# Kernel tuning notes

Hardware: AMD Instinct MI355X
Metric: run time of the kernel (lower is better)

The kernel has to match this reference:

```python
import jax, jax.numpy as jnp
import numpy as np

NOPE = 128          # qk_nope_head_dim
ROPE = 64           # qk_rope_head_dim
KV_LORA = 512       # kv_lora_rank
SCALE = (KV_LORA + ROPE) ** (-0.5)


def setup_inputs() -> dict:
    key = jax.random.key(0)
    k1, k2, k3, k4, k5 = jax.random.split(key, 5)
    T, H, K, S = 512, 128, 512, 8192
    q = jax.random.normal(k1, (T, H, NOPE + ROPE), dtype=jnp.float32)
    kv_cache = jax.random.normal(k2, (S, KV_LORA + ROPE), dtype=jnp.float32)
    topk_indices = jax.random.randint(k3, (T, K), 0, S, dtype=jnp.int32)
    k_b_proj_trans = jax.random.normal(k4, (H, KV_LORA, NOPE), dtype=jnp.float32) * 0.02
    v_b_proj = jax.random.normal(k5, (H, 128, KV_LORA), dtype=jnp.float32) * 0.02
    return {"q": q, "kv_cache": kv_cache, "topk_indices": topk_indices,
            "k_b_proj_trans": k_b_proj_trans, "v_b_proj": v_b_proj}


def reference(q, kv_cache, topk_indices, k_b_proj_trans, v_b_proj):
    # q: [T, H, 192]; kv_cache: [S, 576]; topk_indices: [T, K]
    q_nope, q_rope = q[..., :NOPE], q[..., NOPE:]
    # bmm_out(q_nope_t, k_b_proj_trans.transpose(1,2)): [T,H,128] x [H,512,128] -> [T,H,512]
    q_lat = jnp.einsum('thd,hkd->thk', q_nope, k_b_proj_trans)
    q_concat = jnp.concatenate([q_lat, q_rope], axis=-1)        # [T, H, 576]
    # sparse MLA: gather selected latent KV per token
    kv_sel = kv_cache[topk_indices]                              # [T, K, 576]
    scores = jnp.einsum('thc,tkc->thk', q_concat, kv_sel) * SCALE
    p = jax.nn.softmax(scores, axis=-1)                          # [T, H, K]
    attn_lat = jnp.einsum('thk,tkc->thc', p, kv_sel[..., :KV_LORA])  # [T, H, 512]
    # bmm_out(attn_lat_t, v_b_proj.transpose(1,2)): [T,H,512] x [H,512,128] -> [T,H,128]
    out = jnp.einsum('thc,hvc->thv', attn_lat, v_b_proj)
    return out
```

## Files before the change

### kernel.cpp

```cpp
#include <hip/hip_runtime.h>
#include <stdint.h>


#define SCALE 0.041666666666666664f

typedef __bf16 bf16x8 __attribute__((ext_vector_type(8)));
typedef float floatx4 __attribute__((ext_vector_type(4)));
typedef unsigned int uint32x2 __attribute__((ext_vector_type(2)));
typedef unsigned int uint32x4 __attribute__((ext_vector_type(4)));

static __device__ __forceinline__ unsigned short f2bf(float f) {
  unsigned int u = __builtin_bit_cast(unsigned int, f);
  u += 0x7FFF + ((u >> 16) & 1);
  return (unsigned short)(u >> 16);
}
static __device__ __forceinline__ float bf2f(unsigned short h) {
  unsigned int u = ((unsigned int)h) << 16;
  return __builtin_bit_cast(float, u);
}
static __device__ __forceinline__ unsigned int pack2(float lo, float hi) {
  return (unsigned int)f2bf(lo) | ((unsigned int)f2bf(hi) << 16);
}
static __device__ __forceinline__ void ldsdma16(const void* g, void* l) {
  __builtin_amdgcn_global_load_lds(
      (const __attribute__((address_space(1))) void*)g,
      (__attribute__((address_space(3))) void*)l, 16, 0, 0);
}
static __device__ __forceinline__ void issue_fence() {
  asm volatile("" ::: "memory");
  __builtin_amdgcn_sched_barrier(0);
}
static __device__ __forceinline__ unsigned int lds_addr(const void* p) {
  return (unsigned int)(unsigned long long)(
      (__attribute__((address_space(3))) const void*)p);
}
#define TR64(dst, addr, OFF) \
  asm volatile("ds_read_b64_tr_b16 %0, %1 offset:" OFF : "=v"(dst) : "v"(addr))

static __device__ __forceinline__ void stage8_f32(const float* __restrict__ src,
                                                  unsigned short* dst) {
  const float4* s4 = reinterpret_cast<const float4*>(src);
  float4 v0 = s4[0], v1 = s4[1];
  uint4 o;
  o.x = pack2(v0.x, v0.y); o.y = pack2(v0.z, v0.w);
  o.z = pack2(v1.x, v1.y); o.w = pack2(v1.z, v1.w);
  *reinterpret_cast<uint4*>(dst) = o;
}

static __device__ __forceinline__ void mfma_4x4(const unsigned short* As,
                                                const unsigned short* Bs,
                                                int wm, int wn, int l15, int quad,
                                                floatx4 acc[4][4]) {
  bf16x8 af[4], bfr[4];
#pragma unroll
  for (int i = 0; i < 4; ++i)
    af[i] = *reinterpret_cast<const bf16x8*>(&As[(wm + i * 16 + l15) * 32 + quad * 8]);
#pragma unroll
  for (int j = 0; j < 4; ++j)
    bfr[j] = *reinterpret_cast<const bf16x8*>(&Bs[(wn + j * 16 + l15) * 32 + quad * 8]);
#pragma unroll
  for (int i = 0; i < 4; ++i)
#pragma unroll
    for (int j = 0; j < 4; ++j)
      acc[i][j] = __builtin_amdgcn_mfma_f32_16x16x32_bf16(af[i], bfr[j], acc[i][j], 0, 0, 0);
}

__global__ void prep(const float* __restrict__ kv, unsigned short* __restrict__ kvb,
                     const float* __restrict__ q, unsigned short* __restrict__ qc2) {
  int b = blockIdx.x;
  if (b < 4608) {
    int i = b * 256 + threadIdx.x;
    float4 v = reinterpret_cast<const float4*>(kv)[i];
    ushort4 o;
    o.x = f2bf(v.x); o.y = f2bf(v.y); o.z = f2bf(v.z); o.w = f2bf(v.w);
    reinterpret_cast<ushort4*>(kvb)[i] = o;
  } else {
    int i = (b - 4608) * 256 + threadIdx.x;
    int r = i & 63;
    int th = i >> 6;
    int t = th >> 7, h = th & 127;
    qc2[(((size_t)t * 18 + 16 + (r >> 5)) * 128 + h) * 32 + (r & 31)] =
        f2bf(q[(size_t)th * 192 + 128 + r] * SCALE);
  }
}

__global__ __launch_bounds__(256) void qlat_gemm(const float* __restrict__ q,
                                                 const float* __restrict__ kb,
                                                 unsigned short* __restrict__ qc2) {
  const int h = blockIdx.x;
  const int tm = (blockIdx.y & 3) * 128;
  const int tn = (blockIdx.y >> 2) * 128;
  __shared__ __align__(16) unsigned short As[128 * 32];
  __shared__ __align__(16) unsigned short Bs[128 * 32];
  const int tid = threadIdx.x;
  const int lane = tid & 63, wave = tid >> 6;
  const int wm = (wave & 1) * 64, wn = (wave >> 1) * 64;
  const int l15 = lane & 15, quad = lane >> 4;
  const int r0 = tid >> 2, cg = tid & 3;
  const float* a0 = q + ((size_t)(tm + r0) * 128 + h) * 192 + cg * 8;
  const float* a1 = q + ((size_t)(tm + r0 + 64) * 128 + h) * 192 + cg * 8;
  const float* b0 = kb + ((size_t)h * 512 + tn + r0) * 128 + cg * 8;
  const float* b1 = b0 + (size_t)64 * 128;
  floatx4 acc[4][4] = {};
  for (int ks = 0; ks < 4; ++ks) {
    stage8_f32(a0 + ks * 32, &As[tid * 8]);
    stage8_f32(a1 + ks * 32, &As[2048 + tid * 8]);
    stage8_f32(b0 + ks * 32, &Bs[tid * 8]);
    stage8_f32(b1 + ks * 32, &Bs[2048 + tid * 8]);
    __syncthreads();
    mfma_4x4(As, Bs, wm, wn, l15, quad, acc);
    __syncthreads();
  }
#pragma unroll
  for (int i = 0; i < 4; ++i) {
    const int row = wm + i * 16 + quad * 4;
#pragma unroll
    for (int j = 0; j < 4; ++j) {
      const int c = tn + wn + j * 16 + l15;
      const int ks2 = c >> 5, kk = c & 31;
#pragma unroll
      for (int r = 0; r < 4; ++r) {
        const int t = tm + row + r;
        qc2[(((size_t)t * 18 + ks2) * 128 + h) * 32 + kk] = f2bf(acc[i][j][r] * SCALE);
      }
    }
  }
}

__global__ __launch_bounds__(256) void scores_gemm(const unsigned short* __restrict__ qc2,
                                                   const unsigned short* __restrict__ kvb,
                                                   const int* __restrict__ topk,
                                                   unsigned short* __restrict__ P) {
  const int t = blockIdx.x;
  const int tn = blockIdx.y * 128;
  __shared__ __align__(16) unsigned short Bs[3][128 * 32];
  const int tid = threadIdx.x;
  const int lane = tid & 63, wave = tid >> 6;
  const int wm = (wave & 1) * 64, wn = (wave >> 1) * 64;
  const int l15 = lane & 15, quad = lane >> 4;
  const int r0 = tid >> 2, cg = tid & 3;
  const int idx0 = topk[t * 512 + tn + r0];
  const int idx1 = topk[t * 512 + tn + r0 + 64];
  const unsigned short* b0 = kvb + (size_t)idx0 * 576 + cg * 8;
  const unsigned short* b1 = kvb + (size_t)idx1 * 576 + cg * 8;
  const unsigned short* aab =
      qc2 + ((size_t)t * 2304 + wm + l15) * 32 + quad * 8;
  floatx4 acc[4][4] = {};
  ldsdma16(b0, &Bs[0][tid * 8]);
  ldsdma16(b1, &Bs[0][2048 + tid * 8]);
  ldsdma16(b0 + 32, &Bs[1][tid * 8]);
  ldsdma16(b1 + 32, &Bs[1][2048 + tid * 8]);
  issue_fence();
  bf16x8 af[4], an[4];
#pragma unroll
  for (int i = 0; i < 4; ++i)
    af[i] = *reinterpret_cast<const bf16x8*>(aab + i * 512);
  int bi = 0, bn = 2;
  for (int ks = 0; ks < 18; ++ks) {
    asm volatile("s_waitcnt vmcnt(6)" ::: "memory");
    __builtin_amdgcn_s_barrier();
    if (ks < 16) {
      ldsdma16(b0 + (ks + 2) * 32, &Bs[bn][tid * 8]);
      ldsdma16(b1 + (ks + 2) * 32, &Bs[bn][2048 + tid * 8]);
      issue_fence();
    }
    if (ks < 17) {
#pragma unroll
      for (int i = 0; i < 4; ++i)
        an[i] = *reinterpret_cast<const bf16x8*>(
            aab + (size_t)(ks + 1) * 4096 + i * 512);
    }
    bf16x8 bfr[4];
#pragma unroll
    for (int j = 0; j < 4; ++j)
      bfr[j] = *reinterpret_cast<const bf16x8*>(
          &Bs[bi][(wn + j * 16 + l15) * 32 + quad * 8]);
#pragma unroll
    for (int i = 0; i < 4; ++i)
#pragma unroll
      for (int j = 0; j < 4; ++j)
        acc[i][j] =
            __builtin_amdgcn_mfma_f32_16x16x32_bf16(af[i], bfr[j], acc[i][j], 0, 0, 0);
    __builtin_amdgcn_s_barrier();
#pragma unroll
    for (int i = 0; i < 4; ++i) af[i] = an[i];
    bi = bi == 2 ? 0 : bi + 1;
    bn = bn == 2 ? 0 : bn + 1;
  }
#pragma unroll
  for (int i = 0; i < 4; ++i) {
    const int row = wm + i * 16 + quad * 4;
#pragma unroll
    for (int j = 0; j < 4; ++j) {
      const int col = tn + wn + j * 16 + l15;
#pragma unroll
      for (int r = 0; r < 4; ++r)
        P[((size_t)t * 128 + row + r) * 512 + col] = f2bf(acc[i][j][r]);
    }
  }
}

__global__ __launch_bounds__(256) void softmax_rows(const unsigned short* __restrict__ Pin,
                                                    unsigned short* __restrict__ P2) {
  const int row = blockIdx.x * 4 + (threadIdx.x >> 6);
  const int t = row >> 7, h = row & 127;
  const int lane = threadIdx.x & 63;
  const unsigned short* rp = Pin + (size_t)row * 512 + lane * 8;
  uint4 raw = *reinterpret_cast<const uint4*>(rp);
  unsigned int w[4] = {raw.x, raw.y, raw.z, raw.w};
  float f[8];
  float mx = -1e30f;
#pragma unroll
  for (int i = 0; i < 8; ++i) {
    f[i] = bf2f((unsigned short)((w[i >> 1] >> ((i & 1) * 16)) & 0xFFFF));
    mx = fmaxf(mx, f[i]);
  }
#pragma unroll
  for (int off = 32; off; off >>= 1) mx = fmaxf(mx, __shfl_xor(mx, off, 64));
  float s = 0.f;
#pragma unroll
  for (int i = 0; i < 8; ++i) { f[i] = __expf(f[i] - mx); s += f[i]; }
#pragma unroll
  for (int off = 32; off; off >>= 1) s += __shfl_xor(s, off, 64);
  const float inv = 1.0f / s;
  uint4 o;
  o.x = pack2(f[0] * inv, f[1] * inv);
  o.y = pack2(f[2] * inv, f[3] * inv);
  o.z = pack2(f[4] * inv, f[5] * inv);
  o.w = pack2(f[6] * inv, f[7] * inv);
  unsigned short* wp =
      P2 + (((size_t)t * 16 + (lane >> 2)) * 128 + h) * 32 + (lane & 3) * 8;
  *reinterpret_cast<uint4*>(wp) = o;
}

__global__ __launch_bounds__(512) void attn_gemm(const unsigned short* __restrict__ P2,
                                                 const unsigned short* __restrict__ kvb,
                                                 const int* __restrict__ topk,
                                                 unsigned short* __restrict__ alat2) {
  const int t = blockIdx.x;
  __shared__ __align__(16) unsigned short St[3][32 * 512];
  const int tid = threadIdx.x;
  const int lane = tid & 63, wave = tid >> 6;
  const int wm = (wave >> 2) * 64;
  const int wc = wave & 3;
  const int l15 = lane & 15, quad = lane >> 4;
  const int keyBase = (tid >> 8) * 4 + ((tid >> 1) & 3);
  const int cA = ((tid >> 3) & 31) * 16 + (tid & 1) * 8;
  const int* tkrow = topk + t * 512;
  const unsigned short* a_base =
      P2 + ((size_t)t * 16 * 128 + wm + l15) * 32 + quad * 8;
  const unsigned int tra0 = lds_addr(&St[0][0]) + quad * 8192 + wc * 1024 + l15 * 8;
  floatx4 acc[4][8] = {};
  bf16x8 a_cur[4], a_nxt[4];
  int ip0, ip1, ip2, ip3;
  {
#pragma unroll
    for (int d = 0; d < 4; ++d) {
      const int k0 = tkrow[d * 8 + keyBase];
      ldsdma16(kvb + (size_t)k0 * 576 + cA, &St[0][d * 4096 + tid * 8]);
    }
#pragma unroll
    for (int i = 0; i < 4; ++i)
      a_cur[i] = *reinterpret_cast<const bf16x8*>(a_base + (size_t)i * 16 * 32);
    ip0 = tkrow[64 + 0 * 8 + keyBase];
    ip1 = tkrow[64 + 1 * 8 + keyBase];
    ip2 = tkrow[64 + 2 * 8 + keyBase];
    ip3 = tkrow[64 + 3 * 8 + keyBase];
    issue_fence();
#pragma unroll
    for (int d = 0; d < 4; ++d) {
      const int k1 = tkrow[32 + d * 8 + keyBase];
      ldsdma16(kvb + (size_t)k1 * 576 + cA, &St[1][d * 4096 + tid * 8]);
    }
  }
  int sti = 0, stp = 2;
  for (int ks = 0; ks < 16; ++ks) {
    asm volatile("s_waitcnt vmcnt(4)" ::: "memory");
    __builtin_amdgcn_s_barrier();
    const unsigned int tra = tra0 + sti * 32768;
    uint32x2 rl0, rl1, rl2, rl3, rl4, rl5, rl6, rl7;
    uint32x2 rh0, rh1, rh2, rh3, rh4, rh5, rh6, rh7;
    TR64(rl0, tra, "0");    TR64(rh0, tra, "4096");
    TR64(rl1, tra, "128");  TR64(rh1, tra, "4224");
    TR64(rl2, tra, "256");  TR64(rh2, tra, "4352");
    TR64(rl3, tra, "384");  TR64(rh3, tra, "4480");
    TR64(rl4, tra, "512");  TR64(rh4, tra, "4608");
    TR64(rl5, tra, "640");  TR64(rh5, tra, "4736");
    TR64(rl6, tra, "768");  TR64(rh6, tra, "4864");
    TR64(rl7, tra, "896");  TR64(rh7, tra, "4992");
    if (ks < 15) {
#pragma unroll
      for (int i = 0; i < 4; ++i)
        a_nxt[i] = *reinterpret_cast<const bf16x8*>(
            a_base + ((size_t)(ks + 1) * 128 + i * 16) * 32);
    }
    if (ks < 14) {
      const int d0 = ip0, d1 = ip1, d2 = ip2, d3 = ip3;
      if (ks < 13) {
        ip0 = tkrow[(ks + 3) * 32 + 0 * 8 + keyBase];
        ip1 = tkrow[(ks + 3) * 32 + 1 * 8 + keyBase];
        ip2 = tkrow[(ks + 3) * 32 + 2 * 8 + keyBase];
        ip3 = tkrow[(ks + 3) * 32 + 3 * 8 + keyBase];
      }
      issue_fence();
      ldsdma16(kvb + (size_t)d0 * 576 + cA, &St[stp][0 * 4096 + tid * 8]);
      ldsdma16(kvb + (size_t)d1 * 576 + cA, &St[stp][1 * 4096 + tid * 8]);
      ldsdma16(kvb + (size_t)d2 * 576 + cA, &St[stp][2 * 4096 + tid * 8]);
      ldsdma16(kvb + (size_t)d3 * 576 + cA, &St[stp][3 * 4096 + tid * 8]);
    }
    asm volatile("s_waitcnt lgkmcnt(0)");
    __builtin_amdgcn_sched_barrier(0);
    bf16x8 bfr[8];
    {
      uint32x4 w;
      w.x = rl0.x; w.y = rl0.y; w.z = rh0.x; w.w = rh0.y; bfr[0] = __builtin_bit_cast(bf16x8, w);
      w.x = rl1.x; w.y = rl1.y; w.z = rh1.x; w.w = rh1.y; bfr[1] = __builtin_bit_cast(bf16x8, w);
      w.x = rl2.x; w.y = rl2.y; w.z = rh2.x; w.w = rh2.y; bfr[2] = __builtin_bit_cast(bf16x8, w);
      w.x = rl3.x; w.y = rl3.y; w.z = rh3.x; w.w = rh3.y; bfr[3] = __builtin_bit_cast(bf16x8, w);
      w.x = rl4.x; w.y = rl4.y; w.z = rh4.x; w.w = rh4.y; bfr[4] = __builtin_bit_cast(bf16x8, w);
      w.x = rl5.x; w.y = rl5.y; w.z = rh5.x; w.w = rh5.y; bfr[5] = __builtin_bit_cast(bf16x8, w);
      w.x = rl6.x; w.y = rl6.y; w.z = rh6.x; w.w = rh6.y; bfr[6] = __builtin_bit_cast(bf16x8, w);
      w.x = rl7.x; w.y = rl7.y; w.z = rh7.x; w.w = rh7.y; bfr[7] = __builtin_bit_cast(bf16x8, w);
    }
#pragma unroll
    for (int i = 0; i < 4; ++i)
#pragma unroll
      for (int j = 0; j < 8; ++j)
        acc[i][j] =
            __builtin_amdgcn_mfma_f32_16x16x32_bf16(a_cur[i], bfr[j], acc[i][j], 0, 0, 0);
#pragma unroll
    for (int i = 0; i < 4; ++i) a_cur[i] = a_nxt[i];
    sti = sti == 2 ? 0 : sti + 1;
    stp = stp == 2 ? 0 : stp + 1;
  }
#pragma unroll
  for (int i = 0; i < 4; ++i) {
    const int row = wm + i * 16 + quad * 4;
#pragma unroll
    for (int j = 0; j < 8; ++j) {
      const int c = wc * 128 + j * 16 + l15;
      const int ks2 = c >> 5, kk = c & 31;
#pragma unroll
      for (int r = 0; r < 4; ++r)
        alat2[(((size_t)(row + r) * 16 + ks2) * 512 + t) * 32 + kk] =
            f2bf(acc[i][j][r]);
    }
  }
}

__global__ __launch_bounds__(256) void out_gemm(const unsigned short* __restrict__ alat2,
                                                const float* __restrict__ vb,
                                                float* __restrict__ out) {
  const int h = blockIdx.x;
  const int tm = blockIdx.y * 128;
  __shared__ __align__(16) unsigned short Bs[128 * 32];
  const int tid = threadIdx.x;
  const int lane = tid & 63, wave = tid >> 6;
  const int wm = (wave & 1) * 64, wn = (wave >> 1) * 64;
  const int l15 = lane & 15, quad = lane >> 4;
  const int r0 = tid >> 2, cg = tid & 3;
  const unsigned short* aab =
      alat2 + ((size_t)h * 8192 + tm + wm + l15) * 32 + quad * 8;
  const float* b0 = vb + ((size_t)h * 128 + r0) * 512 + cg * 8;
  const float* b1 = b0 + (size_t)64 * 512;
  floatx4 acc[4][4] = {};
  for (int ks = 0; ks < 16; ++ks) {
    stage8_f32(b0 + ks * 32, &Bs[tid * 8]);
    stage8_f32(b1 + ks * 32, &Bs[2048 + tid * 8]);
    __syncthreads();
    bf16x8 af[4], bfr[4];
#pragma unroll
    for (int i = 0; i < 4; ++i)
      af[i] = *reinterpret_cast<const bf16x8*>(
          aab + (size_t)ks * 16384 + i * 512);
#pragma unroll
    for (int j = 0; j < 4; ++j)
      bfr[j] = *reinterpret_cast<const bf16x8*>(
          &Bs[(wn + j * 16 + l15) * 32 + quad * 8]);
#pragma unroll
    for (int i = 0; i < 4; ++i)
#pragma unroll
      for (int j = 0; j < 4; ++j)
        acc[i][j] =
            __builtin_amdgcn_mfma_f32_16x16x32_bf16(af[i], bfr[j], acc[i][j], 0, 0, 0);
    __syncthreads();
  }
#pragma unroll
  for (int i = 0; i < 4; ++i) {
    const int row = wm + i * 16 + quad * 4;
#pragma unroll
    for (int j = 0; j < 4; ++j) {
      const int col = wn + j * 16 + l15;
#pragma unroll
      for (int r = 0; r < 4; ++r) {
        const int t = tm + row + r;
        out[((size_t)t * 128 + h) * 128 + col] = acc[i][j][r];
      }
    }
  }
}

extern "C" void kernel_launch(void* const* d_in, const int* in_sizes, int n_in,
                              void* d_out, int out_size, void* d_ws, size_t ws_size,
                              hipStream_t stream) {
  const float* q = (const float*)d_in[0];
  const float* kv = (const float*)d_in[1];
  const int* topk = (const int*)d_in[2];
  const float* kb = (const float*)d_in[3];
  const float* vb = (const float*)d_in[4];
  float* out = (float*)d_out;

  char* ws = (char*)d_ws;
  unsigned short* kvb = (unsigned short*)ws;
  unsigned short* qc2 = (unsigned short*)(ws + 9437184);
  unsigned short* P = (unsigned short*)(ws + 9437184 + 75497472);
  unsigned short* P2 = qc2;
  unsigned short* alat2 = P;

  prep<<<dim3(20992), dim3(256), 0, stream>>>(kv, kvb, q, qc2);
  qlat_gemm<<<dim3(128, 16), dim3(256), 0, stream>>>(q, kb, qc2);
  scores_gemm<<<dim3(512, 4), dim3(256), 0, stream>>>(qc2, kvb, topk, P);
  softmax_rows<<<dim3(16384), dim3(256), 0, stream>>>(P, P2);
  attn_gemm<<<dim3(512), dim3(512), 0, stream>>>(P2, kvb, topk, alat2);
  out_gemm<<<dim3(128, 4), dim3(256), 0, stream>>>(alat2, vb, out);
}
```

Measured before the change: 384.6 us.

## Fuse score GEMM with softmax into one per-token kernel

The scores GEMM now uses one 512-thread block per token that covers all 512 selected keys, instead of four 128-key blocks. The row softmax is done in registers, with cross-wave max and sum reductions through small LDS arrays, and the normalized bf16 probabilities are written straight into the layout attn_gemm expects. This removes the separate softmax kernel and the write and re-read of the full bf16 score matrix, and it drops the trailing barrier in the K loop. In exchange it uses about 100KB of LDS per block, doubles the accumulator registers per lane and launches far fewer blocks, which may lower occupancy and latency hiding.

```diff
diff --git a/kernel.cpp b/kernel.cpp
--- a/kernel.cpp
+++ b/kernel.cpp
@@ -127,29 +127,42 @@
   }
 }
 
-__global__ __launch_bounds__(256) void scores_gemm(const unsigned short* __restrict__ qc2,
-                                                   const unsigned short* __restrict__ kvb,
-                                                   const int* __restrict__ topk,
-                                                   unsigned short* __restrict__ P) {
+__global__ __launch_bounds__(512) void scores_fused(const unsigned short* __restrict__ qc2,
+                                                    const unsigned short* __restrict__ kvb,
+                                                    const int* __restrict__ topk,
+                                                    unsigned short* __restrict__ P2) {
   const int t = blockIdx.x;
-  const int tn = blockIdx.y * 128;
-  __shared__ __align__(16) unsigned short Bs[3][128 * 32];
+  __shared__ __align__(16) unsigned short Bs[3][512 * 32];
+  __shared__ __align__(16) float redmx[128][4];
+  __shared__ __align__(16) float redsm[128][4];
   const int tid = threadIdx.x;
   const int lane = tid & 63, wave = tid >> 6;
-  const int wm = (wave & 1) * 64, wn = (wave >> 1) * 64;
+  const int wm2 = (wave >> 2) * 64;
+  const int wkn = (wave & 3) * 128;
   const int l15 = lane & 15, quad = lane >> 4;
-  const int r0 = tid >> 2, cg = tid & 3;
-  const int idx0 = topk[t * 512 + tn + r0];
-  const int idx1 = topk[t * 512 + tn + r0 + 64];
-  const unsigned short* b0 = kvb + (size_t)idx0 * 576 + cg * 8;
-  const unsigned short* b1 = kvb + (size_t)idx1 * 576 + cg * 8;
+  const int keyD = tid >> 2;
+  const int cD = (tid & 3) * 8;
+  const int* tkrow = topk + t * 512;
+  const int gi0 = tkrow[0 * 128 + keyD];
+  const int gi1 = tkrow[1 * 128 + keyD];
+  const int gi2 = tkrow[2 * 128 + keyD];
+  const int gi3 = tkrow[3 * 128 + keyD];
+  const unsigned short* g0 = kvb + (size_t)gi0 * 576 + cD;
+  const unsigned short* g1 = kvb + (size_t)gi1 * 576 + cD;
+  const unsigned short* g2 = kvb + (size_t)gi2 * 576 + cD;
+  const unsigned short* g3 = kvb + (size_t)gi3 * 576 + cD;
   const unsigned short* aab =
-      qc2 + ((size_t)t * 2304 + wm + l15) * 32 + quad * 8;
-  floatx4 acc[4][4] = {};
-  ldsdma16(b0, &Bs[0][tid * 8]);
-  ldsdma16(b1, &Bs[0][2048 + tid * 8]);
-  ldsdma16(b0 + 32, &Bs[1][tid * 8]);
-  ldsdma16(b1 + 32, &Bs[1][2048 + tid * 8]);
+      qc2 + ((size_t)t * 2304 + wm2 + l15) * 32 + quad * 8;
+  floatx4 acc[4][8] = {};
+  ldsdma16(g0, &Bs[0][0 * 4096 + tid * 8]);
+  ldsdma16(g1, &Bs[0][1 * 4096 + tid * 8]);
+  ldsdma16(g2, &Bs[0][2 * 4096 + tid * 8]);
+  ldsdma16(g3, &Bs[0][3 * 4096 + tid * 8]);
+  issue_fence();
+  ldsdma16(g0 + 32, &Bs[1][0 * 4096 + tid * 8]);
+  ldsdma16(g1 + 32, &Bs[1][1 * 4096 + tid * 8]);
+  ldsdma16(g2 + 32, &Bs[1][2 * 4096 + tid * 8]);
+  ldsdma16(g3 + 32, &Bs[1][3 * 4096 + tid * 8]);
   issue_fence();
   bf16x8 af[4], an[4];
 #pragma unroll
@@ -157,11 +170,13 @@
     af[i] = *reinterpret_cast<const bf16x8*>(aab + i * 512);
   int bi = 0, bn = 2;
   for (int ks = 0; ks < 18; ++ks) {
-    asm volatile("s_waitcnt vmcnt(6)" ::: "memory");
+    asm volatile("s_waitcnt vmcnt(8)" ::: "memory");
     __builtin_amdgcn_s_barrier();
     if (ks < 16) {
-      ldsdma16(b0 + (ks + 2) * 32, &Bs[bn][tid * 8]);
-      ldsdma16(b1 + (ks + 2) * 32, &Bs[bn][2048 + tid * 8]);
+      ldsdma16(g0 + (ks + 2) * 32, &Bs[bn][0 * 4096 + tid * 8]);
+      ldsdma16(g1 + (ks + 2) * 32, &Bs[bn][1 * 4096 + tid * 8]);
+      ldsdma16(g2 + (ks + 2) * 32, &Bs[bn][2 * 4096 + tid * 8]);
+      ldsdma16(g3 + (ks + 2) * 32, &Bs[bn][3 * 4096 + tid * 8]);
       issue_fence();
     }
     if (ks < 17) {
@@ -170,67 +185,80 @@
         an[i] = *reinterpret_cast<const bf16x8*>(
             aab + (size_t)(ks + 1) * 4096 + i * 512);
     }
-    bf16x8 bfr[4];
-#pragma unroll
-    for (int j = 0; j < 4; ++j)
+    bf16x8 bfr[8];
+#pragma unroll
+    for (int j = 0; j < 8; ++j)
       bfr[j] = *reinterpret_cast<const bf16x8*>(
-          &Bs[bi][(wn + j * 16 + l15) * 32 + quad * 8]);
+          &Bs[bi][(wkn + j * 16 + l15) * 32 + quad * 8]);
 #pragma unroll
     for (int i = 0; i < 4; ++i)
 #pragma unroll
-      for (int j = 0; j < 4; ++j)
+      for (int j = 0; j < 8; ++j)
         acc[i][j] =
             __builtin_amdgcn_mfma_f32_16x16x32_bf16(af[i], bfr[j], acc[i][j], 0, 0, 0);
-    __builtin_amdgcn_s_barrier();
 #pragma unroll
     for (int i = 0; i < 4; ++i) af[i] = an[i];
     bi = bi == 2 ? 0 : bi + 1;
     bn = bn == 2 ? 0 : bn + 1;
   }
-#pragma unroll
-  for (int i = 0; i < 4; ++i) {
-    const int row = wm + i * 16 + quad * 4;
-#pragma unroll
-    for (int j = 0; j < 4; ++j) {
-      const int col = tn + wn + j * 16 + l15;
-#pragma unroll
-      for (int r = 0; r < 4; ++r)
-        P[((size_t)t * 128 + row + r) * 512 + col] = f2bf(acc[i][j][r]);
-    }
-  }
-}
-
-__global__ __launch_bounds__(256) void softmax_rows(const unsigned short* __restrict__ Pin,
-                                                    unsigned short* __restrict__ P2) {
-  const int row = blockIdx.x * 4 + (threadIdx.x >> 6);
-  const int t = row >> 7, h = row & 127;
-  const int lane = threadIdx.x & 63;
-  const unsigned short* rp = Pin + (size_t)row * 512 + lane * 8;
-  uint4 raw = *reinterpret_cast<const uint4*>(rp);
-  unsigned int w[4] = {raw.x, raw.y, raw.z, raw.w};
-  float f[8];
-  float mx = -1e30f;
-#pragma unroll
-  for (int i = 0; i < 8; ++i) {
-    f[i] = bf2f((unsigned short)((w[i >> 1] >> ((i & 1) * 16)) & 0xFFFF));
-    mx = fmaxf(mx, f[i]);
-  }
-#pragma unroll
-  for (int off = 32; off; off >>= 1) mx = fmaxf(mx, __shfl_xor(mx, off, 64));
-  float s = 0.f;
-#pragma unroll
-  for (int i = 0; i < 8; ++i) { f[i] = __expf(f[i] - mx); s += f[i]; }
-#pragma unroll
-  for (int off = 32; off; off >>= 1) s += __shfl_xor(s, off, 64);
-  const float inv = 1.0f / s;
-  uint4 o;
-  o.x = pack2(f[0] * inv, f[1] * inv);
-  o.y = pack2(f[2] * inv, f[3] * inv);
-  o.z = pack2(f[4] * inv, f[5] * inv);
-  o.w = pack2(f[6] * inv, f[7] * inv);
-  unsigned short* wp =
-      P2 + (((size_t)t * 16 + (lane >> 2)) * 128 + h) * 32 + (lane & 3) * 8;
-  *reinterpret_cast<uint4*>(wp) = o;
+  float fm[4][4], inv[4][4];
+#pragma unroll
+  for (int i = 0; i < 4; ++i)
+#pragma unroll
+    for (int r = 0; r < 4; ++r) {
+      float m = acc[i][0][r];
+#pragma unroll
+      for (int j = 1; j < 8; ++j) m = fmaxf(m, acc[i][j][r]);
+#pragma unroll
+      for (int off = 1; off <= 8; off <<= 1) m = fmaxf(m, __shfl_xor(m, off, 64));
+      if (l15 == 0) redmx[wm2 + i * 16 + quad * 4 + r][wave & 3] = m;
+    }
+  __syncthreads();
+#pragma unroll
+  for (int i = 0; i < 4; ++i)
+#pragma unroll
+    for (int r = 0; r < 4; ++r) {
+      const float4 q4 =
+          *reinterpret_cast<const float4*>(redmx[wm2 + i * 16 + quad * 4 + r]);
+      fm[i][r] = fmaxf(fmaxf(q4.x, q4.y), fmaxf(q4.z, q4.w));
+    }
+#pragma unroll
+  for (int i = 0; i < 4; ++i)
+#pragma unroll
+    for (int r = 0; r < 4; ++r) {
+      float s = 0.f;
+#pragma unroll
+      for (int j = 0; j < 8; ++j) {
+        const float e = __expf(acc[i][j][r] - fm[i][r]);
+        acc[i][j][r] = e;
+        s += e;
+      }
+#pragma unroll
+      for (int off = 1; off <= 8; off <<= 1) s += __shfl_xor(s, off, 64);
+      if (l15 == 0) redsm[wm2 + i * 16 + quad * 4 + r][wave & 3] = s;
+    }
+  __syncthreads();
+#pragma unroll
+  for (int i = 0; i < 4; ++i)
+#pragma unroll
+    for (int r = 0; r < 4; ++r) {
+      const float4 q4 =
+          *reinterpret_cast<const float4*>(redsm[wm2 + i * 16 + quad * 4 + r]);
+      inv[i][r] = 1.0f / (q4.x + q4.y + q4.z + q4.w);
+    }
+#pragma unroll
+  for (int i = 0; i < 4; ++i)
+#pragma unroll
+    for (int j = 0; j < 8; ++j) {
+      const int ks2 = (wave & 3) * 4 + (j >> 1);
+      const int co = (j & 1) * 16 + l15;
+#pragma unroll
+      for (int r = 0; r < 4; ++r) {
+        const int head = wm2 + i * 16 + quad * 4 + r;
+        P2[(((size_t)t * 16 + ks2) * 128 + head) * 32 + co] =
+            f2bf(acc[i][j][r] * inv[i][r]);
+      }
+    }
 }
 
 __global__ __launch_bounds__(512) void attn_gemm(const unsigned short* __restrict__ P2,
@@ -413,14 +441,12 @@
   char* ws = (char*)d_ws;
   unsigned short* kvb = (unsigned short*)ws;
   unsigned short* qc2 = (unsigned short*)(ws + 9437184);
-  unsigned short* P = (unsigned short*)(ws + 9437184 + 75497472);
-  unsigned short* P2 = qc2;
-  unsigned short* alat2 = P;
+  unsigned short* P2 = (unsigned short*)(ws + 9437184 + 75497472);
+  unsigned short* alat2 = qc2;
 
   prep<<<dim3(20992), dim3(256), 0, stream>>>(kv, kvb, q, qc2);
   qlat_gemm<<<dim3(128, 16), dim3(256), 0, stream>>>(q, kb, qc2);
-  scores_gemm<<<dim3(512, 4), dim3(256), 0, stream>>>(qc2, kvb, topk, P);
-  softmax_rows<<<dim3(16384), dim3(256), 0, stream>>>(P, P2);
+  scores_fused<<<dim3(512), dim3(512), 0, stream>>>(qc2, kvb, topk, P2);
   attn_gemm<<<dim3(512), dim3(512), 0, stream>>>(P2, kvb, topk, alat2);
   out_gemm<<<dim3(128, 4), dim3(256), 0, stream>>>(alat2, vb, out);
 }
```

New measurement: 361.9 us. 5.9% less time.
